# Performance work log

Measured on AMD Instinct MI355X. Metric: run time of the kernel, lower is better.

## Reference

```python
import jax, jax.numpy as jnp
import numpy as np

N_NODES = 200000
N_EDGES = 6400000
IN_CH = 128
HID = 16
NUM_CLASSES = 16
NUM_GRAPHS = 512


def _gcn_conv(x, W, b, src, dst, n_nodes):
    """PyG GCNConv: h = x @ W; out = D^{-1/2}(A+I)D^{-1/2} h + b (self-loops added)."""
    loop = jnp.arange(n_nodes, dtype=src.dtype)
    s = jnp.concatenate([src, loop])
    d = jnp.concatenate([dst, loop])
    # degree of A + I (counting incoming edges at dst, plus self loop)
    deg = jax.ops.segment_sum(jnp.ones_like(d, dtype=x.dtype), d, num_segments=n_nodes)
    dinv = jnp.where(deg > 0, jax.lax.rsqrt(deg), 0.0)
    norm = dinv[s] * dinv[d]  # [E + N]
    h = x @ W  # [N, out] -- transform before propagate (small feature dim)
    msg = norm[:, None] * h[s]  # gather over edges
    out = jax.ops.segment_sum(msg, d, num_segments=n_nodes)  # scatter-add
    return out + b


def _global_mean_pool(x, batch, num_graphs):
    s = jax.ops.segment_sum(x, batch, num_segments=num_graphs, indices_are_sorted=True)
    cnt = jax.ops.segment_sum(jnp.ones((x.shape[0],), x.dtype), batch,
                              num_segments=num_graphs, indices_are_sorted=True)
    return s / jnp.maximum(cnt, 1.0)[:, None]


def setup_inputs() -> dict:
    key = jax.random.key(0)
    ks = jax.random.split(key, 8)
    x = jax.random.normal(ks[0], (N_NODES, IN_CH), dtype=jnp.float32)
    edge_index = jax.random.randint(ks[1], (2, N_EDGES), 0, N_NODES, dtype=jnp.int64)
    batch = jnp.sort(jax.random.randint(ks[2], (N_NODES,), 0, NUM_GRAPHS, dtype=jnp.int64))
    W1 = jax.random.normal(ks[3], (IN_CH, HID), dtype=jnp.float32) / np.sqrt(IN_CH)
    b1 = jnp.zeros((HID,), jnp.float32)
    W2 = jax.random.normal(ks[4], (HID, HID), dtype=jnp.float32) / np.sqrt(HID)
    b2 = jnp.zeros((HID,), jnp.float32)
    fc_W = jax.random.normal(ks[5], (HID, NUM_CLASSES), dtype=jnp.float32) / np.sqrt(HID)
    fc_b = jnp.zeros((NUM_CLASSES,), jnp.float32)
    return {"x": x, "W1": W1, "b1": b1, "W2": W2, "b2": b2,
            "fc_W": fc_W, "fc_b": fc_b, "edge_index": edge_index,
            "batch": batch, "num_graphs": NUM_GRAPHS}


def reference(x, W1, b1, W2, b2, fc_W, fc_b, edge_index, batch, num_graphs):
    n_nodes = x.shape[0]
    src, dst = edge_index[0], edge_index[1]
    h = _gcn_conv(x, W1, b1, src, dst, n_nodes)
    h = jax.nn.relu(h)
    h = _gcn_conv(h, W2, b2, src, dst, n_nodes)
    g = _global_mean_pool(h, batch, num_graphs)  # [num_graphs, HID]
    return g @ fc_W + fc_b  # [num_graphs, num_classes]
```

## Files before the change

### kernel.cpp

```cpp
#include <hip/hip_runtime.h>

#define TPB 256
#define BSH 9
#define BNODES (1 << BSH)
#define BMASK (BNODES - 1)
#define SCAT_TPB 1024
#define STILE 16384
#define EPT 16
#define SORT_TPB 1024
#define QCAP 6144
#define CAP 18432

typedef _Float16 half8 __attribute__((ext_vector_type(8)));
typedef _Float16 half2v __attribute__((ext_vector_type(2)));

__global__ void k_init(int* __restrict__ gpos, float* __restrict__ gsum,
                       int nbuck, int gsum_len) {
  int i = blockIdx.x * blockDim.x + threadIdx.x;
  if (i < nbuck) gpos[i] = i * CAP;
  if (i < gsum_len) gsum[i] = 0.0f;
}

__global__ void __launch_bounds__(SCAT_TPB)
k_scat(const int* __restrict__ src, const int* __restrict__ dst,
       int* __restrict__ gpos, unsigned* __restrict__ bucketed,
       int E, int nbuck) {
  __shared__ unsigned stage[STILE];
  __shared__ int cnt[512];
  __shared__ int runp[512];
  __shared__ int lofs[513];
  __shared__ int base[512];
  __shared__ int wsum[16];
  int t = threadIdx.x;
  int ts = blockIdx.x * STILE;
  int count = min(STILE, E - ts);
  int d[EPT], s[EPT];

  for (int i = t; i < nbuck; i += SCAT_TPB) cnt[i] = 0;
  __syncthreads();
#pragma unroll
  for (int j = 0; j < EPT; ++j) {
    int i = j * SCAT_TPB + t;
    if (i < count) {
      d[j] = dst[ts + i];
      s[j] = src[ts + i];
      atomicAdd(&cnt[d[j] >> BSH], 1);
    }
  }
  __syncthreads();
  {
    int v = (t < nbuck) ? cnt[t] : 0;
    int lane = t & 63, wid = t >> 6;
    int inc = v;
    for (int dd = 1; dd < 64; dd <<= 1) {
      int u = __shfl_up(inc, dd, 64);
      if (lane >= dd) inc += u;
    }
    if (lane == 63) wsum[wid] = inc;
    __syncthreads();
    int woff = 0;
    for (int w = 0; w < wid; ++w) woff += wsum[w];
    int excl = woff + inc - v;
    if (t < nbuck) {
      lofs[t] = excl;
      runp[t] = excl;
      base[t] = v ? atomicAdd(&gpos[t], v) : 0;
    }
    if (t == 0) lofs[nbuck] = count;
  }
  __syncthreads();
#pragma unroll
  for (int j = 0; j < EPT; ++j) {
    int i = j * SCAT_TPB + t;
    if (i < count) {
      int b = d[j] >> BSH;
      int p = atomicAdd(&runp[b], 1);
      stage[p] = ((unsigned)(d[j] & BMASK) << 18) | (unsigned)s[j];
    }
  }
  __syncthreads();
  {
    int lane = t & 63, wid = t >> 6;
    for (int b = wid; b < nbuck; b += SCAT_TPB / 64) {
      int s0 = lofs[b], s1 = lofs[b + 1];
      int gb = base[b];
      for (int i = s0 + lane; i < s1; i += 64)
        bucketed[gb + (i - s0)] = stage[i];
    }
  }
}

__global__ void __launch_bounds__(SORT_TPB)
k_sortb(const unsigned* __restrict__ bucketed, const int* __restrict__ gpos,
        int* __restrict__ csr, int* __restrict__ off, int* __restrict__ endo,
        float* __restrict__ dinv, int halfN, int N) {
  int b = blockIdx.x;
  int t = threadIdx.x;
  int n0 = b << BSH;
  int beg = b * CAP;
  int end = gpos[b];
  int total = end - beg;
  __shared__ int cntT[BNODES];
  __shared__ int cntA[BNODES];
  __shared__ int runA[BNODES];
  __shared__ int runB[BNODES];
  __shared__ int wsum[16];
  __shared__ unsigned stage[QCAP];
  __shared__ int qinfo[2];
  if (t < BNODES) { cntT[t] = 0; cntA[t] = 0; }
  __syncthreads();
  for (int i = beg + t; i < end; i += SORT_TPB) {
    unsigned p = bucketed[i];
    int idx = (p >> 18) & BMASK;
    atomicAdd(&cntT[idx], 1);
    if ((int)(p & 0x3ffffu) < halfN) atomicAdd(&cntA[idx], 1);
  }
  __syncthreads();
  int v = (t < BNODES) ? cntT[t] : 0;
  int lane = t & 63, wid = t >> 6;
  int inc = v;
  for (int d = 1; d < 64; d <<= 1) {
    int u = __shfl_up(inc, d, 64);
    if (lane >= d) inc += u;
  }
  if (lane == 63) wsum[wid] = inc;
  __syncthreads();
  int woff = 0;
  for (int w = 0; w < wid; ++w) woff += wsum[w];
  int excl = woff + inc - v;
  if (t < BNODES) {
    runA[t] = excl;
    runB[t] = excl + cntA[t];
    int n = n0 + t;
    if (n < N) {
      off[n] = beg + excl;
      endo[n] = beg + excl + v;
      dinv[n] = rsqrtf((float)v + 1.0f);
    }
  }
  __syncthreads();
  for (int q = 0; q < 4; ++q) {
    if (t == 0) {
      qinfo[0] = runA[q << 7];
      qinfo[1] = (q < 3) ? runA[(q + 1) << 7] : total;
    }
    __syncthreads();
    int qs = qinfo[0];
    int qcnt = qinfo[1] - qs;
    for (int i = beg + t; i < end; i += SORT_TPB) {
      unsigned p = bucketed[i];
      int idx = (p >> 18) & BMASK;
      if ((idx >> 7) == q) {
        bool low = (int)(p & 0x3ffffu) < halfN;
        int r = atomicAdd(low ? &runA[idx] : &runB[idx], 1);
        int pos = r - qs;
        if (pos < QCAP) stage[pos] = p & 0x3ffffu;
        else csr[beg + r] = (int)(p & 0x3ffffu);
      }
    }
    __syncthreads();
    int lim = qcnt < QCAP ? qcnt : QCAP;
    for (int i = t; i < lim; i += SORT_TPB)
      csr[beg + qs + i] = (int)stage[i];
    __syncthreads();
  }
}

__global__ void k_xw1(const float* __restrict__ x, const float* __restrict__ W1,
                      const float* __restrict__ dinv, _Float16* __restrict__ hs,
                      int n_nodes) {
  int n = blockIdx.x * blockDim.x + threadIdx.x;
  if (n >= n_nodes) return;
  const float4* xr = reinterpret_cast<const float4*>(x + (size_t)n * 128);
  float s[16];
#pragma unroll
  for (int c = 0; c < 16; ++c) s[c] = 0.0f;
#pragma unroll 4
  for (int k4 = 0; k4 < 32; ++k4) {
    float4 xv = xr[k4];
    const float* w = W1 + k4 * 64;
#pragma unroll
    for (int c = 0; c < 16; ++c) s[c] = fmaf(xv.x, w[c], s[c]);
#pragma unroll
    for (int c = 0; c < 16; ++c) s[c] = fmaf(xv.y, w[16 + c], s[c]);
#pragma unroll
    for (int c = 0; c < 16; ++c) s[c] = fmaf(xv.z, w[32 + c], s[c]);
#pragma unroll
    for (int c = 0; c < 16; ++c) s[c] = fmaf(xv.w, w[48 + c], s[c]);
  }
  float dn = dinv[n];
  half8 v0, v1;
#pragma unroll
  for (int j = 0; j < 8; ++j) v0[j] = (_Float16)(dn * s[j]);
#pragma unroll
  for (int j = 0; j < 8; ++j) v1[j] = (_Float16)(dn * s[8 + j]);
  half8* hp = reinterpret_cast<half8*>(hs + (size_t)n * 16);
  hp[0] = v0;
  hp[1] = v1;
}

__device__ __forceinline__ void gather2(const _Float16* __restrict__ tab,
                                        const int* __restrict__ csr,
                                        int beg, int end, int c2,
                                        float& a0, float& a1) {
  int i = beg;
  for (; i + 8 <= end; i += 8) {
    half2v f[8];
#pragma unroll
    for (int j = 0; j < 8; ++j) {
      int idx = csr[i + j];
      f[j] = *reinterpret_cast<const half2v*>(tab + (size_t)idx * 16 + c2 * 2);
    }
#pragma unroll
    for (int j = 0; j < 8; ++j) { a0 += (float)f[j][0]; a1 += (float)f[j][1]; }
  }
  for (; i < end; ++i) {
    int idx = csr[i];
    half2v f = *reinterpret_cast<const half2v*>(tab + (size_t)idx * 16 + c2 * 2);
    a0 += (float)f[0];
    a1 += (float)f[1];
  }
}

__global__ void k_gc1(const _Float16* __restrict__ hs1, const int* __restrict__ off,
                      const int* __restrict__ endo, const int* __restrict__ csr,
                      const float* __restrict__ dinv, const float* __restrict__ b1,
                      const float* __restrict__ W2, _Float16* __restrict__ hs2, int N) {
  int t = blockIdx.x * blockDim.x + threadIdx.x;
  int n = t >> 3, c2 = t & 7;
  if (n >= N) return;
  half2v selfr = *reinterpret_cast<const half2v*>(hs1 + (size_t)n * 16 + c2 * 2);
  float a0 = (float)selfr[0], a1 = (float)selfr[1];
  gather2(hs1, csr, off[n], endo[n], c2, a0, a1);
  float dn = dinv[n];
  float h1a = fmaxf(fmaf(dn, a0, b1[c2 * 2 + 0]), 0.0f);
  float h1b = fmaxf(fmaf(dn, a1, b1[c2 * 2 + 1]), 0.0f);
  float oa = 0.0f, ob = 0.0f;
#pragma unroll
  for (int j = 0; j < 8; ++j) {
    float hk0 = __shfl(h1a, j, 8);
    float hk1 = __shfl(h1b, j, 8);
    oa = fmaf(hk0, W2[(2 * j) * 16 + c2 * 2 + 0], oa);
    ob = fmaf(hk0, W2[(2 * j) * 16 + c2 * 2 + 1], ob);
    oa = fmaf(hk1, W2[(2 * j + 1) * 16 + c2 * 2 + 0], oa);
    ob = fmaf(hk1, W2[(2 * j + 1) * 16 + c2 * 2 + 1], ob);
  }
  half2v outv;
  outv[0] = (_Float16)(dn * oa);
  outv[1] = (_Float16)(dn * ob);
  *reinterpret_cast<half2v*>(hs2 + (size_t)n * 16 + c2 * 2) = outv;
}

__global__ void k_gc2(const _Float16* __restrict__ hs2, const int* __restrict__ off,
                      const int* __restrict__ endo, const int* __restrict__ csr,
                      const float* __restrict__ dinv, const float* __restrict__ b2,
                      const int* __restrict__ batch, float* __restrict__ gsum, int N) {
  int t = threadIdx.x;
  int n = blockIdx.x * 32 + (t >> 3);
  int c2 = t & 7;
  float v0 = 0.0f, v1 = 0.0f;
  int g = 0;
  if (n < N) {
    half2v selfr = *reinterpret_cast<const half2v*>(hs2 + (size_t)n * 16 + c2 * 2);
    float a0 = (float)selfr[0], a1 = (float)selfr[1];
    gather2(hs2, csr, off[n], endo[n], c2, a0, a1);
    float dn = dinv[n];
    v0 = fmaf(dn, a0, b2[c2 * 2 + 0]);
    v1 = fmaf(dn, a1, b2[c2 * 2 + 1]);
    g = batch[n];
  }
  __shared__ float2 red[256];
  __shared__ int sg[2];
  int nfirst = blockIdx.x * 32;
  int nlast = min(nfirst + 31, N - 1);
  if (t == 0) sg[0] = batch[nfirst];
  if (t == 255) sg[1] = batch[nlast];
  __syncthreads();
  bool uniform = (sg[0] == sg[1]);
  if (uniform) {
    red[t] = make_float2(v0, v1);
    __syncthreads();
#pragma unroll
    for (int s2 = 16; s2 > 0; s2 >>= 1) {
      if ((t >> 3) < s2) {
        float2 a = red[t], b = red[t + s2 * 8];
        red[t] = make_float2(a.x + b.x, a.y + b.y);
      }
      __syncthreads();
    }
    if (t < 8) {
      float2 r = red[t];
      unsafeAtomicAdd(&gsum[(size_t)sg[0] * 16 + t * 2 + 0], r.x);
      unsafeAtomicAdd(&gsum[(size_t)sg[0] * 16 + t * 2 + 1], r.y);
    }
  } else if (n < N) {
    unsafeAtomicAdd(&gsum[(size_t)g * 16 + c2 * 2 + 0], v0);
    unsafeAtomicAdd(&gsum[(size_t)g * 16 + c2 * 2 + 1], v1);
  }
}

__device__ __forceinline__ int lbound(const int* a, int n, int key) {
  int lo = 0, hi = n;
  while (lo < hi) {
    int mid = (lo + hi) >> 1;
    if (a[mid] < key) lo = mid + 1; else hi = mid;
  }
  return lo;
}

__global__ void k_final(const float* __restrict__ gsum, const int* __restrict__ batch,
                        const float* __restrict__ fcW, const float* __restrict__ fcb,
                        float* __restrict__ out, int n_nodes, int num_graphs) {
  int g = blockIdx.x * blockDim.x + threadIdx.x;
  if (g >= num_graphs) return;
  int lo = lbound(batch, n_nodes, g);
  int hi = lbound(batch, n_nodes, g + 1);
  float cnt = (float)(hi - lo);
  float inv = 1.0f / fmaxf(cnt, 1.0f);
  float gv[16];
#pragma unroll
  for (int c = 0; c < 16; ++c) gv[c] = gsum[(size_t)g * 16 + c] * inv;
  float o[16];
#pragma unroll
  for (int c = 0; c < 16; ++c) o[c] = fcb[c];
#pragma unroll
  for (int k = 0; k < 16; ++k) {
    float gk = gv[k];
    const float* w = fcW + k * 16;
#pragma unroll
    for (int c = 0; c < 16; ++c) o[c] = fmaf(gk, w[c], o[c]);
  }
#pragma unroll
  for (int c = 0; c < 16; ++c) out[(size_t)g * 16 + c] = o[c];
}

extern "C" void kernel_launch(void* const* d_in, const int* in_sizes, int n_in,
                              void* d_out, int out_size, void* d_ws, size_t ws_size,
                              hipStream_t stream) {
  const float* x   = (const float*)d_in[0];
  const float* W1  = (const float*)d_in[1];
  const float* b1  = (const float*)d_in[2];
  const float* W2  = (const float*)d_in[3];
  const float* b2  = (const float*)d_in[4];
  const float* fcW = (const float*)d_in[5];
  const float* fcb = (const float*)d_in[6];
  const int* ei    = (const int*)d_in[7];
  const int* batch = (const int*)d_in[8];

  const int IN_CH = 128, HID = 16, NCLS = 16;
  int n_nodes = in_sizes[0] / IN_CH;
  int E = in_sizes[7] / 2;
  int num_graphs = out_size / NCLS;
  const int* src = ei;
  const int* dst = ei + E;
  int nbuck = (n_nodes + BNODES - 1) >> BSH;
  int halfN = n_nodes >> 1;
  size_t seg_elems = (size_t)nbuck * CAP;

  char* ws = (char*)d_ws;
  size_t h_bytes = sizeof(_Float16) * (size_t)n_nodes * 16;
  size_t region_bytes = 2 * h_bytes;
  if (sizeof(unsigned) * seg_elems > region_bytes)
    region_bytes = sizeof(unsigned) * seg_elems;
  unsigned* bucketed = (unsigned*)ws;
  _Float16* H1  = (_Float16*)ws;
  _Float16* H2  = (_Float16*)(ws + h_bytes);
  ws += region_bytes;
  int*   csr  = (int*)ws;   ws += sizeof(int) * seg_elems;
  int*   off  = (int*)ws;   ws += sizeof(int) * ((size_t)n_nodes + 64);
  int*   endo = (int*)ws;   ws += sizeof(int) * ((size_t)n_nodes + 64);
  float* dinv = (float*)ws; ws += sizeof(float) * (size_t)n_nodes;
  int*   gpos = (int*)ws;   ws += sizeof(int) * 1056;
  float* gsum = (float*)ws;

  int gn  = (n_nodes + TPB - 1) / TPB;
  int gg  = (num_graphs + TPB - 1) / TPB;
  int gnc = ((n_nodes * 8) + TPB - 1) / TPB;
  int gb  = (n_nodes + 31) / 32;
  int gs  = (E + STILE - 1) / STILE;
  int gi  = ((nbuck > num_graphs * HID ? nbuck : num_graphs * HID) + TPB - 1) / TPB;

  k_init <<<gi, TPB, 0, stream>>>(gpos, gsum, nbuck, num_graphs * HID);
  k_scat <<<gs, SCAT_TPB, 0, stream>>>(src, dst, gpos, bucketed, E, nbuck);
  k_sortb<<<nbuck, SORT_TPB, 0, stream>>>(bucketed, gpos, csr, off, endo,
                                          dinv, halfN, n_nodes);
  k_xw1  <<<gn, TPB, 0, stream>>>(x, W1, dinv, H1, n_nodes);
  k_gc1  <<<gnc, TPB, 0, stream>>>(H1, off, endo, csr, dinv, b1, W2, H2, n_nodes);
  k_gc2  <<<gb, TPB, 0, stream>>>(H2, off, endo, csr, dinv, b2, batch, gsum, n_nodes);
  k_final<<<gg, TPB, 0, stream>>>(gsum, batch, fcW, fcb, (float*)d_out,
                                  n_nodes, num_graphs);
}
```

Baseline: 250.2 us.

## Split neighbor gathers by source half to shrink per-pass gather working set

The sort kernel already orders each node's edges into low-half and high-half source ranges and now records the boundary (mido). Each GCN layer's gather is split into two kernels: one gathers from low-half sources and stores fp32 partials (layer 1) or adds straight into the pooled sums (layer 2), and the other gathers from the high-half sources and finishes the layer. Each pass therefore touches only half of the feature table, so it fits better in cache. CSR index reads and streaming writes also switch to nontemporal hints. In exchange there are extra launches, a partial-sum buffer round trip, and a second pass over the CSR offsets.

```diff
diff --git a/kernel.cpp b/kernel.cpp
--- a/kernel.cpp
+++ b/kernel.cpp
@@ -13,6 +13,7 @@
 
 typedef _Float16 half8 __attribute__((ext_vector_type(8)));
 typedef _Float16 half2v __attribute__((ext_vector_type(2)));
+typedef float float2v __attribute__((ext_vector_type(2)));
 
 __global__ void k_init(int* __restrict__ gpos, float* __restrict__ gsum,
                        int nbuck, int gsum_len) {
@@ -92,8 +93,8 @@
 
 __global__ void __launch_bounds__(SORT_TPB)
 k_sortb(const unsigned* __restrict__ bucketed, const int* __restrict__ gpos,
-        int* __restrict__ csr, int* __restrict__ off, int* __restrict__ endo,
-        float* __restrict__ dinv, int halfN, int N) {
+        int* __restrict__ csr, int* __restrict__ off, int* __restrict__ mido,
+        int* __restrict__ endo, float* __restrict__ dinv, int halfN, int N) {
   int b = blockIdx.x;
   int t = threadIdx.x;
   int n0 = b << BSH;
@@ -134,6 +135,7 @@
     int n = n0 + t;
     if (n < N) {
       off[n] = beg + excl;
+      mido[n] = beg + excl + cntA[t];
       endo[n] = beg + excl + v;
       dinv[n] = rsqrtf((float)v + 1.0f);
     }
@@ -208,30 +210,51 @@
     half2v f[8];
 #pragma unroll
     for (int j = 0; j < 8; ++j) {
-      int idx = csr[i + j];
+      int idx = __builtin_nontemporal_load(csr + i + j);
       f[j] = *reinterpret_cast<const half2v*>(tab + (size_t)idx * 16 + c2 * 2);
     }
 #pragma unroll
     for (int j = 0; j < 8; ++j) { a0 += (float)f[j][0]; a1 += (float)f[j][1]; }
   }
   for (; i < end; ++i) {
-    int idx = csr[i];
+    int idx = __builtin_nontemporal_load(csr + i);
     half2v f = *reinterpret_cast<const half2v*>(tab + (size_t)idx * 16 + c2 * 2);
     a0 += (float)f[0];
     a1 += (float)f[1];
   }
 }
 
-__global__ void k_gc1(const _Float16* __restrict__ hs1, const int* __restrict__ off,
-                      const int* __restrict__ endo, const int* __restrict__ csr,
-                      const float* __restrict__ dinv, const float* __restrict__ b1,
-                      const float* __restrict__ W2, _Float16* __restrict__ hs2, int N) {
+__global__ void k_gc1a(const _Float16* __restrict__ hs1, const int* __restrict__ off,
+                       const int* __restrict__ mido, const int* __restrict__ csr,
+                       float* __restrict__ part, int N) {
   int t = blockIdx.x * blockDim.x + threadIdx.x;
   int n = t >> 3, c2 = t & 7;
   if (n >= N) return;
-  half2v selfr = *reinterpret_cast<const half2v*>(hs1 + (size_t)n * 16 + c2 * 2);
+  float a0 = 0.0f, a1 = 0.0f;
+  gather2(hs1, csr, off[n], mido[n], c2, a0, a1);
+  float2v v;
+  v[0] = a0;
+  v[1] = a1;
+  __builtin_nontemporal_store(
+      v, reinterpret_cast<float2v*>(part + (size_t)n * 16 + c2 * 2));
+}
+
+__global__ void k_gc1b(const _Float16* __restrict__ hs1, const int* __restrict__ mido,
+                       const int* __restrict__ endo, const int* __restrict__ csr,
+                       const float* __restrict__ part, const float* __restrict__ dinv,
+                       const float* __restrict__ b1, const float* __restrict__ W2,
+                       _Float16* __restrict__ hs2, int N) {
+  int t = blockIdx.x * blockDim.x + threadIdx.x;
+  int n = t >> 3, c2 = t & 7;
+  if (n >= N) return;
+  half2v selfr = __builtin_nontemporal_load(
+      reinterpret_cast<const half2v*>(hs1 + (size_t)n * 16 + c2 * 2));
   float a0 = (float)selfr[0], a1 = (float)selfr[1];
-  gather2(hs1, csr, off[n], endo[n], c2, a0, a1);
+  gather2(hs1, csr, mido[n], endo[n], c2, a0, a1);
+  float2v pv = __builtin_nontemporal_load(
+      reinterpret_cast<const float2v*>(part + (size_t)n * 16 + c2 * 2));
+  a0 += pv[0];
+  a1 += pv[1];
   float dn = dinv[n];
   float h1a = fmaxf(fmaf(dn, a0, b1[c2 * 2 + 0]), 0.0f);
   float h1b = fmaxf(fmaf(dn, a1, b1[c2 * 2 + 1]), 0.0f);
@@ -248,22 +271,71 @@
   half2v outv;
   outv[0] = (_Float16)(dn * oa);
   outv[1] = (_Float16)(dn * ob);
-  *reinterpret_cast<half2v*>(hs2 + (size_t)n * 16 + c2 * 2) = outv;
-}
-
-__global__ void k_gc2(const _Float16* __restrict__ hs2, const int* __restrict__ off,
-                      const int* __restrict__ endo, const int* __restrict__ csr,
-                      const float* __restrict__ dinv, const float* __restrict__ b2,
-                      const int* __restrict__ batch, float* __restrict__ gsum, int N) {
+  __builtin_nontemporal_store(
+      outv, reinterpret_cast<half2v*>(hs2 + (size_t)n * 16 + c2 * 2));
+}
+
+__global__ void k_gc2a(const _Float16* __restrict__ hs2, const int* __restrict__ off,
+                       const int* __restrict__ mido, const int* __restrict__ csr,
+                       const float* __restrict__ dinv, const int* __restrict__ batch,
+                       float* __restrict__ gsum, int N) {
   int t = threadIdx.x;
   int n = blockIdx.x * 32 + (t >> 3);
   int c2 = t & 7;
   float v0 = 0.0f, v1 = 0.0f;
   int g = 0;
   if (n < N) {
-    half2v selfr = *reinterpret_cast<const half2v*>(hs2 + (size_t)n * 16 + c2 * 2);
+    float a0 = 0.0f, a1 = 0.0f;
+    gather2(hs2, csr, off[n], mido[n], c2, a0, a1);
+    float dn = dinv[n];
+    v0 = dn * a0;
+    v1 = dn * a1;
+    g = batch[n];
+  }
+  __shared__ float2 red[256];
+  __shared__ int sg[2];
+  int nfirst = blockIdx.x * 32;
+  int nlast = min(nfirst + 31, N - 1);
+  if (t == 0) sg[0] = batch[nfirst];
+  if (t == 255) sg[1] = batch[nlast];
+  __syncthreads();
+  bool uniform = (sg[0] == sg[1]);
+  if (uniform) {
+    red[t] = make_float2(v0, v1);
+    __syncthreads();
+#pragma unroll
+    for (int s2 = 16; s2 > 0; s2 >>= 1) {
+      if ((t >> 3) < s2) {
+        float2 a = red[t], b = red[t + s2 * 8];
+        red[t] = make_float2(a.x + b.x, a.y + b.y);
+      }
+      __syncthreads();
+    }
+    if (t < 8) {
+      float2 r = red[t];
+      unsafeAtomicAdd(&gsum[(size_t)sg[0] * 16 + t * 2 + 0], r.x);
+      unsafeAtomicAdd(&gsum[(size_t)sg[0] * 16 + t * 2 + 1], r.y);
+    }
+  } else if (n < N) {
+    unsafeAtomicAdd(&gsum[(size_t)g * 16 + c2 * 2 + 0], v0);
+    unsafeAtomicAdd(&gsum[(size_t)g * 16 + c2 * 2 + 1], v1);
+  }
+}
+
+__global__ void k_gc2b(const _Float16* __restrict__ hs2, const int* __restrict__ mido,
+                       const int* __restrict__ endo, const int* __restrict__ csr,
+                       const float* __restrict__ dinv, const float* __restrict__ b2,
+                       const int* __restrict__ batch, float* __restrict__ gsum, int N) {
+  int t = threadIdx.x;
+  int n = blockIdx.x * 32 + (t >> 3);
+  int c2 = t & 7;
+  float v0 = 0.0f, v1 = 0.0f;
+  int g = 0;
+  if (n < N) {
+    half2v selfr = __builtin_nontemporal_load(
+        reinterpret_cast<const half2v*>(hs2 + (size_t)n * 16 + c2 * 2));
     float a0 = (float)selfr[0], a1 = (float)selfr[1];
-    gather2(hs2, csr, off[n], endo[n], c2, a0, a1);
+    gather2(hs2, csr, mido[n], endo[n], c2, a0, a1);
     float dn = dinv[n];
     v0 = fmaf(dn, a0, b2[c2 * 2 + 0]);
     v1 = fmaf(dn, a1, b2[c2 * 2 + 1]);
@@ -359,15 +431,18 @@
 
   char* ws = (char*)d_ws;
   size_t h_bytes = sizeof(_Float16) * (size_t)n_nodes * 16;
-  size_t region_bytes = 2 * h_bytes;
+  size_t part_bytes = sizeof(float) * (size_t)n_nodes * 16;
+  size_t region_bytes = 2 * h_bytes + part_bytes;
   if (sizeof(unsigned) * seg_elems > region_bytes)
     region_bytes = sizeof(unsigned) * seg_elems;
   unsigned* bucketed = (unsigned*)ws;
   _Float16* H1  = (_Float16*)ws;
   _Float16* H2  = (_Float16*)(ws + h_bytes);
+  float*    part = (float*)(ws + 2 * h_bytes);
   ws += region_bytes;
   int*   csr  = (int*)ws;   ws += sizeof(int) * seg_elems;
   int*   off  = (int*)ws;   ws += sizeof(int) * ((size_t)n_nodes + 64);
+  int*   mido = (int*)ws;   ws += sizeof(int) * ((size_t)n_nodes + 64);
   int*   endo = (int*)ws;   ws += sizeof(int) * ((size_t)n_nodes + 64);
   float* dinv = (float*)ws; ws += sizeof(float) * (size_t)n_nodes;
   int*   gpos = (int*)ws;   ws += sizeof(int) * 1056;
@@ -382,11 +457,15 @@
 
   k_init <<<gi, TPB, 0, stream>>>(gpos, gsum, nbuck, num_graphs * HID);
   k_scat <<<gs, SCAT_TPB, 0, stream>>>(src, dst, gpos, bucketed, E, nbuck);
-  k_sortb<<<nbuck, SORT_TPB, 0, stream>>>(bucketed, gpos, csr, off, endo,
+  k_sortb<<<nbuck, SORT_TPB, 0, stream>>>(bucketed, gpos, csr, off, mido, endo,
                                           dinv, halfN, n_nodes);
   k_xw1  <<<gn, TPB, 0, stream>>>(x, W1, dinv, H1, n_nodes);
-  k_gc1  <<<gnc, TPB, 0, stream>>>(H1, off, endo, csr, dinv, b1, W2, H2, n_nodes);
-  k_gc2  <<<gb, TPB, 0, stream>>>(H2, off, endo, csr, dinv, b2, batch, gsum, n_nodes);
+  k_gc1a <<<gnc, TPB, 0, stream>>>(H1, off, mido, csr, part, n_nodes);
+  k_gc1b <<<gnc, TPB, 0, stream>>>(H1, mido, endo, csr, part, dinv, b1, W2, H2,
+                                   n_nodes);
+  k_gc2a <<<gb, TPB, 0, stream>>>(H2, off, mido, csr, dinv, batch, gsum, n_nodes);
+  k_gc2b <<<gb, TPB, 0, stream>>>(H2, mido, endo, csr, dinv, b2, batch, gsum,
+                                  n_nodes);
   k_final<<<gg, TPB, 0, stream>>>(gsum, batch, fcW, fcb, (float*)d_out,
                                   n_nodes, num_graphs);
 }
```

After: 317.4 us. +26.9%, slower.
